# Optimization experiments

Hardware: AMD Instinct MI355X
Metric: run time of the kernel (lower is better)

Reference implementation:

```python
import jax, jax.numpy as jnp
import numpy as np

N = 100000
E = 3200000
NFEAT = 256
NHID = 256
NCLASS = 40


def _uniform(key, shape, stdv):
    return jax.random.uniform(key, shape, jnp.float32, -stdv, stdv)


def setup_inputs() -> dict:
    key = jax.random.key(0)
    ks = jax.random.split(key, 16)
    x = jax.random.normal(ks[0], (N, NFEAT), jnp.float32)
    edge_row = jax.random.randint(ks[1], (E,), 0, N, jnp.int32)
    edge_col = jax.random.randint(ks[2], (E,), 0, N, jnp.int32)
    edge_weight = jax.random.uniform(ks[3], (E,), jnp.float32)
    # MyLinear init: stdv = 1/sqrt(out_features)
    dims = [(NFEAT, NHID), (NHID, NHID), (NHID, NHID), (NHID, NCLASS)]
    params = {}
    for i, (fi, fo) in enumerate(dims):
        stdv = 1.0 / np.sqrt(fo)
        params[f"W{i+1}"] = _uniform(ks[4 + 2 * i], (fi, fo), stdv)
        params[f"b{i+1}"] = _uniform(ks[5 + 2 * i], (fo,), stdv)
    return dict(x=x, edge_row=edge_row, edge_col=edge_col, edge_weight=edge_weight, **params)


def _spmm(edge_row, edge_col, edge_weight, x):
    # out[i] = sum_{(i,j) in E} w_ij * x[j]
    msgs = edge_weight[:, None] * x[edge_col]  # [E, d]
    return jax.ops.segment_sum(msgs, edge_row, num_segments=N)


def reference(x, edge_row, edge_col, edge_weight, W1, b1, W2, b2, W3, b3, W4, b4):
    # layer 0 (ix % mlp_layers == 0 -> residual + spmm)
    h = x + _spmm(edge_row, edge_col, edge_weight, x)
    h = jax.nn.relu(h @ W1 + b1)
    # layer 1
    h = jax.nn.relu(h @ W2 + b2)
    # layer 2 (spmm + residual again)
    h = h + _spmm(edge_row, edge_col, edge_weight, h)
    h = jax.nn.relu(h @ W3 + b3)
    # layer 3 (final, no relu)
    h = h @ W4 + b4
    return jax.nn.log_softmax(h, axis=1)
```

## Files before the change

### kernel.cpp

```cpp
#include <hip/hip_runtime.h>
#include <hip/hip_bf16.h>
#include <cstdint>

#define N_NODES 100000
#define N_EDGES 3200000
#define NFEAT   256
#define NCLASS  40

#define BROWS_LOG 7
#define BROWS     128
#define NBUCK     782
#define CHUNK     8192
#define NBLK      391
#define GHN       (NBUCK * NBLK)

typedef __bf16 bf16;
typedef __attribute__((ext_vector_type(8))) __bf16 bf16x8;
typedef __attribute__((ext_vector_type(4))) float f32x4;
typedef __attribute__((ext_vector_type(2))) float f32x2;

__device__ inline float b2f(unsigned short u) {
    union { unsigned int i; float f; } x; x.i = ((unsigned int)u) << 16; return x.f;
}
__device__ inline unsigned short f2b(float f) {
    union { float f; unsigned int i; } x; x.f = f;
    unsigned int i = x.i;
    return (unsigned short)((i + 0x7fffu + ((i >> 16) & 1u)) >> 16);
}
__device__ inline f32x2 unpack2(unsigned int d) {
    union { unsigned int i; float f; } lo, hi;
    lo.i = d << 16;
    hi.i = d & 0xFFFF0000u;
    return (f32x2){lo.f, hi.f};
}
__device__ inline unsigned int pack2(f32x2 a) {
    return ((unsigned int)f2b(a[0])) | (((unsigned int)f2b(a[1])) << 16);
}

__global__ void prep_w_kernel(const float* __restrict__ W1, const float* __restrict__ W2,
                              const float* __restrict__ W3, const float* __restrict__ W4,
                              unsigned short* __restrict__ WT1, unsigned short* __restrict__ WT2,
                              unsigned short* __restrict__ WT3, unsigned short* __restrict__ WT4) {
    int i = blockIdx.x * blockDim.x + threadIdx.x;
    if (i < 256 * 256) {
        int nIdx = i >> 8, k = i & 255;
        WT1[i] = f2b(W1[k * 256 + nIdx]);
        WT2[i] = f2b(W2[k * 256 + nIdx]);
        WT3[i] = f2b(W3[k * 256 + nIdx]);
    }
    if (i < 48 * 256) {
        int nIdx = i >> 8, k = i & 255;
        WT4[i] = (nIdx < NCLASS) ? f2b(W4[k * NCLASS + nIdx]) : (unsigned short)0;
    }
}

__global__ void cast_kernel(const float* __restrict__ X, unsigned short* __restrict__ Y, int n4) {
    int i = blockIdx.x * blockDim.x + threadIdx.x;
    if (i >= n4) return;
    float4 v = *(const float4*)(X + (size_t)i * 4);
    ushort4 o;
    o.x = f2b(v.x); o.y = f2b(v.y); o.z = f2b(v.z); o.w = f2b(v.w);
    *(ushort4*)(Y + (size_t)i * 4) = o;
}

__global__ __launch_bounds__(256) void p1a_kernel(const int* __restrict__ erow,
                                                  int* __restrict__ ghist) {
    __shared__ int h[NBUCK];
    for (int j = threadIdx.x; j < NBUCK; j += 256) h[j] = 0;
    __syncthreads();
    int base = blockIdx.x * CHUNK;
    for (int j = 0; j < CHUNK; j += 256) {
        int i = base + j + threadIdx.x;
        if (i < N_EDGES) atomicAdd(&h[erow[i] >> BROWS_LOG], 1);
    }
    __syncthreads();
    for (int j = threadIdx.x; j < NBUCK; j += 256)
        ghist[(size_t)j * NBLK + blockIdx.x] = h[j];
}

__global__ void scanB_blocks_kernel(int* __restrict__ g, int* __restrict__ bsums, int n) {
    __shared__ int s[1024];
    int i = blockIdx.x * 1024 + threadIdx.x;
    int v = (i < n) ? g[i] : 0;
    s[threadIdx.x] = v;
    __syncthreads();
    for (int off = 1; off < 1024; off <<= 1) {
        int t = (threadIdx.x >= off) ? s[threadIdx.x - off] : 0;
        __syncthreads();
        s[threadIdx.x] += t;
        __syncthreads();
    }
    if (i < n) g[i] = s[threadIdx.x] - v;
    if (threadIdx.x == 1023) bsums[blockIdx.x] = s[1023];
}

__global__ void scanB_sums_kernel(int* __restrict__ bsums, int nb) {
    __shared__ int s[512];
    int v = (threadIdx.x < nb) ? bsums[threadIdx.x] : 0;
    s[threadIdx.x] = v;
    __syncthreads();
    for (int off = 1; off < 512; off <<= 1) {
        int t = (threadIdx.x >= off) ? s[threadIdx.x - off] : 0;
        __syncthreads();
        s[threadIdx.x] += t;
        __syncthreads();
    }
    if (threadIdx.x < nb) bsums[threadIdx.x] = s[threadIdx.x] - v;
}

__global__ void scanB_add_kernel(int* __restrict__ g, const int* __restrict__ bsums, int n) {
    int i = blockIdx.x * blockDim.x + threadIdx.x;
    if (i < n) g[i] += bsums[i >> 10];
}

__global__ __launch_bounds__(256) void p1c_kernel(const int* __restrict__ erow,
                                                  const int* __restrict__ ecol,
                                                  const float* __restrict__ ew,
                                                  const int* __restrict__ ghist,
                                                  uint2* __restrict__ stage) {
    __shared__ int cur[NBUCK];
    for (int j = threadIdx.x; j < NBUCK; j += 256)
        cur[j] = ghist[(size_t)j * NBLK + blockIdx.x];
    __syncthreads();
    int base = blockIdx.x * CHUNK;
    for (int j = 0; j < CHUNK; j += 1024) {
        int r[4], c[4]; float w[4]; bool m[4];
#pragma unroll
        for (int q = 0; q < 4; q++) {
            int i = base + j + q * 256 + threadIdx.x;
            m[q] = (i < N_EDGES);
            if (m[q]) { r[q] = erow[i]; c[q] = ecol[i]; w[q] = ew[i]; }
        }
#pragma unroll
        for (int q = 0; q < 4; q++) {
            if (m[q]) {
                unsigned int qq = (unsigned int)(w[q] * 32768.f + 0.5f);
                if (qq > 32767u) qq = 32767u;
                int p = atomicAdd(&cur[r[q] >> BROWS_LOG], 1);
                stage[p] = make_uint2((unsigned int)r[q], (((unsigned int)c[q]) << 15) | qq);
            }
        }
    }
}

__global__ __launch_bounds__(256) void p2_kernel(const int* __restrict__ ghist,
                                                 const uint2* __restrict__ stage,
                                                 unsigned int* __restrict__ edges,
                                                 int* __restrict__ rowptr) {
    __shared__ int h[BROWS], sc[BROWS], lcur[BROWS];
    int b = blockIdx.x;
    int lo = ghist[(size_t)b * NBLK];
    int hi = (b + 1 < NBUCK) ? ghist[(size_t)(b + 1) * NBLK] : N_EDGES;
    if (threadIdx.x < BROWS) h[threadIdx.x] = 0;
    __syncthreads();
    for (int i = lo + threadIdx.x; i < hi; i += 256)
        atomicAdd(&h[stage[i].x & (BROWS - 1)], 1);
    __syncthreads();
    if (threadIdx.x < BROWS) sc[threadIdx.x] = h[threadIdx.x];
    __syncthreads();
    for (int off = 1; off < BROWS; off <<= 1) {
        int t = 0;
        if (threadIdx.x < BROWS && threadIdx.x >= off) t = sc[threadIdx.x - off];
        __syncthreads();
        if (threadIdx.x < BROWS) sc[threadIdx.x] += t;
        __syncthreads();
    }
    if (threadIdx.x < BROWS) {
        int ex = sc[threadIdx.x] - h[threadIdx.x];
        int row = b * BROWS + threadIdx.x;
        if (row <= N_NODES) rowptr[row] = lo + ex;
        lcur[threadIdx.x] = lo + ex;
    }
    __syncthreads();
    for (int i = lo + threadIdx.x; i < hi; i += 256) {
        uint2 sd = stage[i];
        int p = atomicAdd(&lcur[sd.x & (BROWS - 1)], 1);
        edges[p] = sd.y;
    }
}

__global__ void spmm_res_kernel(const unsigned short* __restrict__ X, unsigned short* __restrict__ Y,
                                const int* __restrict__ rowptr, const unsigned int* __restrict__ edges,
                                int n) {
    int gtid = blockIdx.x * blockDim.x + threadIdx.x;
    int row = gtid >> 6;
    int lane = gtid & 63;
    if (row >= n) return;
    const int half = lane >> 5;
    const int fb = (lane & 31) * 8;

    f32x2 acc[4];
    {
        uint4 xb = *(const uint4*)(X + (size_t)row * NFEAT + fb);
        if (half == 0) {
            acc[0] = unpack2(xb.x); acc[1] = unpack2(xb.y);
            acc[2] = unpack2(xb.z); acc[3] = unpack2(xb.w);
        } else {
            acc[0] = (f32x2){0.f, 0.f}; acc[1] = (f32x2){0.f, 0.f};
            acc[2] = (f32x2){0.f, 0.f}; acc[3] = (f32x2){0.f, 0.f};
        }
    }

    int s = rowptr[row], e = rowptr[row + 1];
    for (int k = s; k < e; k += 12) {
        int   c[6];
        f32x2 w2[6];
#pragma unroll
        for (int j = 0; j < 6; j++) {
            int kj = k + j * 2 + half;
            int kc = (kj < e) ? kj : (e - 1);
            unsigned int d = edges[kc];
            c[j] = (int)(d >> 15);
            float w = (kj < e) ? (float)(d & 32767u) * (1.f / 32768.f) : 0.f;
            w2[j] = (f32x2){w, w};
        }
        uint4 v[6];
#pragma unroll
        for (int j = 0; j < 6; j++) v[j] = *(const uint4*)(X + (size_t)c[j] * NFEAT + fb);
#pragma unroll
        for (int j = 0; j < 6; j++) {
            acc[0] += w2[j] * unpack2(v[j].x);
            acc[1] += w2[j] * unpack2(v[j].y);
            acc[2] += w2[j] * unpack2(v[j].z);
            acc[3] += w2[j] * unpack2(v[j].w);
        }
    }

#pragma unroll
    for (int i = 0; i < 4; i++) {
        acc[i][0] += __shfl_xor(acc[i][0], 32, 64);
        acc[i][1] += __shfl_xor(acc[i][1], 32, 64);
    }
    if (half == 0) {
        uint4 o;
        o.x = pack2(acc[0]); o.y = pack2(acc[1]);
        o.z = pack2(acc[2]); o.w = pack2(acc[3]);
        *(uint4*)(Y + (size_t)row * NFEAT + fb) = o;
    }
}

template <int NT>
__global__ __launch_bounds__(256) void gemm_relu_kernel(
    const bf16* __restrict__ X, const bf16* __restrict__ WT,
    const float* __restrict__ bias,
    unsigned short* __restrict__ Y, int M) {
    constexpr int NROWS = NT * 16;
    __shared__ unsigned int sB[NROWS * 20];
    const int tid = threadIdx.x;
    const int wave = tid >> 6;
    const int lane = tid & 63;
    const int m = lane & 15;
    const int quad = lane >> 4;
    const int rowBase = blockIdx.x * 64 + wave * 16;
    int arow = rowBase + m;
    if (arow >= M) arow = M - 1;

    f32x4 acc[NT];
#pragma unroll
    for (int t = 0; t < NT; t++) acc[t] = (f32x4){0.f, 0.f, 0.f, 0.f};

    const bf16* xp = X + (size_t)arow * NFEAT + quad * 8;
#pragma unroll
    for (int k0 = 0; k0 < NFEAT; k0 += 32) {
#pragma unroll
        for (int f = tid; f < NROWS * 4; f += 256) {
            int n = f >> 2, j = f & 3;
            uint4 v = *(const uint4*)(WT + (size_t)n * NFEAT + k0 + j * 8);
            *(uint4*)&sB[n * 20 + j * 4] = v;
        }
        __syncthreads();
        bf16x8 a = *(const bf16x8*)(xp + k0);
#pragma unroll
        for (int t = 0; t < NT; t++) {
            bf16x8 b = *(const bf16x8*)&sB[(t * 16 + m) * 20 + quad * 4];
            acc[t] = __builtin_amdgcn_mfma_f32_16x16x32_bf16(a, b, acc[t], 0, 0, 0);
        }
        __syncthreads();
    }

#pragma unroll
    for (int t = 0; t < NT; t++) {
        int col = t * 16 + m;
        float bv = bias[col];
#pragma unroll
        for (int r = 0; r < 4; r++) {
            int row = rowBase + quad * 4 + r;
            if (row < M) {
                float v = fmaxf(acc[t][r] + bv, 0.f);
                Y[(size_t)row * NFEAT + col] = f2b(v);
            }
        }
    }
}

__global__ __launch_bounds__(256) void gemm_ls_kernel(
    const bf16* __restrict__ X, const bf16* __restrict__ WT,
    const float* __restrict__ bias,
    float* __restrict__ out, int M) {
    constexpr int NT = 3;
    constexpr int NROWS = NT * 16;
    __shared__ unsigned int sB[NROWS * 20];
    const int tid = threadIdx.x;
    const int wave = tid >> 6;
    const int lane = tid & 63;
    const int m = lane & 15;
    const int quad = lane >> 4;
    const int rowBase = blockIdx.x * 64 + wave * 16;
    int arow = rowBase + m;
    if (arow >= M) arow = M - 1;

    f32x4 acc[NT];
#pragma unroll
    for (int t = 0; t < NT; t++) acc[t] = (f32x4){0.f, 0.f, 0.f, 0.f};

    const bf16* xp = X + (size_t)arow * NFEAT + quad * 8;
#pragma unroll
    for (int k0 = 0; k0 < NFEAT; k0 += 32) {
        if (tid < NROWS * 4) {
            int n = tid >> 2, j = tid & 3;
            uint4 v = *(const uint4*)(WT + (size_t)n * NFEAT + k0 + j * 8);
            *(uint4*)&sB[n * 20 + j * 4] = v;
        }
        __syncthreads();
        bf16x8 a = *(const bf16x8*)(xp + k0);
#pragma unroll
        for (int t = 0; t < NT; t++) {
            bf16x8 b = *(const bf16x8*)&sB[(t * 16 + m) * 20 + quad * 4];
            acc[t] = __builtin_amdgcn_mfma_f32_16x16x32_bf16(a, b, acc[t], 0, 0, 0);
        }
        __syncthreads();
    }

    float v[3][4];
    bool valid[3];
#pragma unroll
    for (int t = 0; t < 3; t++) {
        int col = t * 16 + m;
        valid[t] = (col < NCLASS);
        float bv = valid[t] ? bias[col] : 0.f;
#pragma unroll
        for (int r = 0; r < 4; r++) v[t][r] = acc[t][r] + bv;
    }

#pragma unroll
    for (int r = 0; r < 4; r++) {
        int row = rowBase + quad * 4 + r;
        float mx = -1e30f;
#pragma unroll
        for (int t = 0; t < 3; t++) if (valid[t]) mx = fmaxf(mx, v[t][r]);
#pragma unroll
        for (int off = 1; off < 16; off <<= 1) mx = fmaxf(mx, __shfl_xor(mx, off, 64));
        float sm = 0.f;
#pragma unroll
        for (int t = 0; t < 3; t++) if (valid[t]) sm += __expf(v[t][r] - mx);
#pragma unroll
        for (int off = 1; off < 16; off <<= 1) sm += __shfl_xor(sm, off, 64);
        float ls = __logf(sm);
        if (row < M) {
#pragma unroll
            for (int t = 0; t < 3; t++) {
                int col = t * 16 + m;
                if (col < NCLASS)
                    out[(size_t)row * NCLASS + col] = v[t][r] - mx - ls;
            }
        }
    }
}

extern "C" void kernel_launch(void* const* d_in, const int* in_sizes, int n_in,
                              void* d_out, int out_size, void* d_ws, size_t ws_size,
                              hipStream_t stream) {
    const float* x   = (const float*)d_in[0];
    const int* erow  = (const int*)d_in[1];
    const int* ecol  = (const int*)d_in[2];
    const float* ew  = (const float*)d_in[3];
    const float* W1  = (const float*)d_in[4];
    const float* W2  = (const float*)d_in[6];
    const float* W3  = (const float*)d_in[8];
    const float* W4  = (const float*)d_in[10];
    const float* b1  = (const float*)d_in[5];
    const float* b2  = (const float*)d_in[7];
    const float* b3  = (const float*)d_in[9];
    const float* b4  = (const float*)d_in[11];

    char* ws = (char*)d_ws;
    size_t off = 0;
    auto alloc = [&](size_t bytes) -> char* {
        char* p = ws + off;
        off = (off + bytes + 255) & ~(size_t)255;
        return p;
    };
    int* rowptr  = (int*)alloc((size_t)(N_NODES + 1) * 4);
    int* bsumsB  = (int*)alloc(512 * 4);
    unsigned int* edges = (unsigned int*)alloc((size_t)N_EDGES * 4);
    int* ghist   = (int*)alloc((size_t)GHN * 4);
    unsigned short* WT1 = (unsigned short*)alloc(256 * 256 * 2);
    unsigned short* WT2 = (unsigned short*)alloc(256 * 256 * 2);
    unsigned short* WT3 = (unsigned short*)alloc(256 * 256 * 2);
    unsigned short* WT4 = (unsigned short*)alloc(48 * 256 * 2);
    unsigned short* hA  = (unsigned short*)alloc((size_t)N_NODES * NFEAT * 2);
    uint2* stage        = (uint2*)hA;
    unsigned short* hB  = (unsigned short*)d_in[0];
    (void)ws_size; (void)n_in; (void)in_sizes; (void)out_size;

    prep_w_kernel<<<(256 * 256 + 255) / 256, 256, 0, stream>>>(
        W1, W2, W3, W4, WT1, WT2, WT3, WT4);
    p1a_kernel<<<NBLK, 256, 0, stream>>>(erow, ghist);
    int nsb = (GHN + 1023) / 1024;
    scanB_blocks_kernel<<<nsb, 1024, 0, stream>>>(ghist, bsumsB, GHN);
    scanB_sums_kernel<<<1, 512, 0, stream>>>(bsumsB, nsb);
    scanB_add_kernel<<<(GHN + 255) / 256, 256, 0, stream>>>(ghist, bsumsB, GHN);
    p1c_kernel<<<NBLK, 256, 0, stream>>>(erow, ecol, ew, ghist, stage);
    p2_kernel<<<NBUCK, 256, 0, stream>>>(ghist, stage, edges, rowptr);

    const int n4 = N_NODES * NFEAT / 4;
    const int spmm_grid = (N_NODES * 64 + 255) / 256;
    const int gemm_grid = (N_NODES + 63) / 64;

    cast_kernel<<<(n4 + 255) / 256, 256, 0, stream>>>(x, hA, n4);
    spmm_res_kernel<<<spmm_grid, 256, 0, stream>>>(hA, hB, rowptr, edges, N_NODES);
    gemm_relu_kernel<16><<<gemm_grid, 256, 0, stream>>>(
        (const bf16*)hB, (const bf16*)WT1, b1, hB, N_NODES);
    gemm_relu_kernel<16><<<gemm_grid, 256, 0, stream>>>(
        (const bf16*)hB, (const bf16*)WT2, b2, hB, N_NODES);
    spmm_res_kernel<<<spmm_grid, 256, 0, stream>>>(hB, hA, rowptr, edges, N_NODES);
    gemm_relu_kernel<16><<<gemm_grid, 256, 0, stream>>>(
        (const bf16*)hA, (const bf16*)WT3, b3, hA, N_NODES);
    gemm_ls_kernel<<<gemm_grid, 256, 0, stream>>>(
        (const bf16*)hA, (const bf16*)WT4, b4, (float*)d_out, N_NODES);
}
```

Before: 969.6 us.

## Fuse SpMM gather with subsequent GEMM layers via shared-memory tiles

Merges each SpMM-with-residual with its following dense layers into one kernel. Each 64-row block gathers neighbor features into LDS, then runs the MFMA GEMMs from LDS and keeps the intermediate activations there. This removes global writes and reads of full activation matrices and four kernel launches. The gather now runs 16 rows sequentially per wave, and the larger LDS footprint lowers occupancy, which may reduce latency hiding for the random gathers.

```diff
diff --git a/kernel.cpp b/kernel.cpp
--- a/kernel.cpp
+++ b/kernel.cpp
@@ -13,6 +13,8 @@
 #define CHUNK     8192
 #define NBLK      391
 #define GHN       (NBUCK * NBLK)
+
+#define SAP 264
 
 typedef __bf16 bf16;
 typedef __attribute__((ext_vector_type(8))) __bf16 bf16x8;
@@ -179,112 +181,137 @@
     }
 }
 
-__global__ void spmm_res_kernel(const unsigned short* __restrict__ X, unsigned short* __restrict__ Y,
-                                const int* __restrict__ rowptr, const unsigned int* __restrict__ edges,
-                                int n) {
-    int gtid = blockIdx.x * blockDim.x + threadIdx.x;
-    int row = gtid >> 6;
-    int lane = gtid & 63;
-    if (row >= n) return;
+
+__device__ __forceinline__ void gather64(
+    const unsigned short* __restrict__ X,
+    const int* __restrict__ rowptr,
+    const unsigned int* __restrict__ edges,
+    unsigned short* __restrict__ sA,
+    int blockRow, int M, int wave, int lane)
+{
     const int half = lane >> 5;
     const int fb = (lane & 31) * 8;
-
-    f32x2 acc[4];
-    {
-        uint4 xb = *(const uint4*)(X + (size_t)row * NFEAT + fb);
-        if (half == 0) {
-            acc[0] = unpack2(xb.x); acc[1] = unpack2(xb.y);
-            acc[2] = unpack2(xb.z); acc[3] = unpack2(xb.w);
-        } else {
-            acc[0] = (f32x2){0.f, 0.f}; acc[1] = (f32x2){0.f, 0.f};
-            acc[2] = (f32x2){0.f, 0.f}; acc[3] = (f32x2){0.f, 0.f};
-        }
-    }
-
-    int s = rowptr[row], e = rowptr[row + 1];
-    for (int k = s; k < e; k += 12) {
-        int   c[6];
-        f32x2 w2[6];
-#pragma unroll
-        for (int j = 0; j < 6; j++) {
-            int kj = k + j * 2 + half;
-            int kc = (kj < e) ? kj : (e - 1);
-            unsigned int d = edges[kc];
-            c[j] = (int)(d >> 15);
-            float w = (kj < e) ? (float)(d & 32767u) * (1.f / 32768.f) : 0.f;
-            w2[j] = (f32x2){w, w};
-        }
-        uint4 v[6];
-#pragma unroll
-        for (int j = 0; j < 6; j++) v[j] = *(const uint4*)(X + (size_t)c[j] * NFEAT + fb);
-#pragma unroll
-        for (int j = 0; j < 6; j++) {
-            acc[0] += w2[j] * unpack2(v[j].x);
-            acc[1] += w2[j] * unpack2(v[j].y);
-            acc[2] += w2[j] * unpack2(v[j].z);
-            acc[3] += w2[j] * unpack2(v[j].w);
-        }
-    }
-
-#pragma unroll
-    for (int i = 0; i < 4; i++) {
-        acc[i][0] += __shfl_xor(acc[i][0], 32, 64);
-        acc[i][1] += __shfl_xor(acc[i][1], 32, 64);
-    }
-    if (half == 0) {
-        uint4 o;
-        o.x = pack2(acc[0]); o.y = pack2(acc[1]);
-        o.z = pack2(acc[2]); o.w = pack2(acc[3]);
-        *(uint4*)(Y + (size_t)row * NFEAT + fb) = o;
-    }
-}
-
-template <int NT>
-__global__ __launch_bounds__(256) void gemm_relu_kernel(
-    const bf16* __restrict__ X, const bf16* __restrict__ WT,
-    const float* __restrict__ bias,
-    unsigned short* __restrict__ Y, int M) {
-    constexpr int NROWS = NT * 16;
-    __shared__ unsigned int sB[NROWS * 20];
-    const int tid = threadIdx.x;
-    const int wave = tid >> 6;
-    const int lane = tid & 63;
-    const int m = lane & 15;
-    const int quad = lane >> 4;
-    const int rowBase = blockIdx.x * 64 + wave * 16;
-    int arow = rowBase + m;
-    if (arow >= M) arow = M - 1;
-
-    f32x4 acc[NT];
-#pragma unroll
-    for (int t = 0; t < NT; t++) acc[t] = (f32x4){0.f, 0.f, 0.f, 0.f};
-
-    const bf16* xp = X + (size_t)arow * NFEAT + quad * 8;
+    for (int lr = 0; lr < 16; ++lr) {
+        const int lrow = wave * 16 + lr;
+        const int row = blockRow + lrow;
+        if (row < M) {
+            f32x2 acc[4];
+            uint4 xb = *(const uint4*)(X + (size_t)row * NFEAT + fb);
+            if (half == 0) {
+                acc[0] = unpack2(xb.x); acc[1] = unpack2(xb.y);
+                acc[2] = unpack2(xb.z); acc[3] = unpack2(xb.w);
+            } else {
+                acc[0] = (f32x2){0.f, 0.f}; acc[1] = (f32x2){0.f, 0.f};
+                acc[2] = (f32x2){0.f, 0.f}; acc[3] = (f32x2){0.f, 0.f};
+            }
+            int s = rowptr[row], e = rowptr[row + 1];
+            for (int k = s; k < e; k += 12) {
+                int   c[6];
+                f32x2 w2[6];
+#pragma unroll
+                for (int j = 0; j < 6; j++) {
+                    int kj = k + j * 2 + half;
+                    int kc = (kj < e) ? kj : (e - 1);
+                    unsigned int d = edges[kc];
+                    c[j] = (int)(d >> 15);
+                    float w = (kj < e) ? (float)(d & 32767u) * (1.f / 32768.f) : 0.f;
+                    w2[j] = (f32x2){w, w};
+                }
+                uint4 v[6];
+#pragma unroll
+                for (int j = 0; j < 6; j++) v[j] = *(const uint4*)(X + (size_t)c[j] * NFEAT + fb);
+#pragma unroll
+                for (int j = 0; j < 6; j++) {
+                    acc[0] += w2[j] * unpack2(v[j].x);
+                    acc[1] += w2[j] * unpack2(v[j].y);
+                    acc[2] += w2[j] * unpack2(v[j].z);
+                    acc[3] += w2[j] * unpack2(v[j].w);
+                }
+            }
+#pragma unroll
+            for (int i = 0; i < 4; i++) {
+                acc[i][0] += __shfl_xor(acc[i][0], 32, 64);
+                acc[i][1] += __shfl_xor(acc[i][1], 32, 64);
+            }
+            if (half == 0) {
+                uint4 o;
+                o.x = pack2(acc[0]); o.y = pack2(acc[1]);
+                o.z = pack2(acc[2]); o.w = pack2(acc[3]);
+                *(uint4*)&sA[lrow * SAP + fb] = o;
+            }
+        } else if (half == 0) {
+            uint4 z; z.x = 0u; z.y = 0u; z.z = 0u; z.w = 0u;
+            *(uint4*)&sA[lrow * SAP + fb] = z;
+        }
+    }
+}
+
+__device__ __forceinline__ void gemm256(
+    const unsigned short* __restrict__ sA,
+    unsigned int* __restrict__ sB,
+    const unsigned short* __restrict__ WT,
+    f32x4 acc[16], int wave, int m, int quad, int tid)
+{
+#pragma unroll
+    for (int t = 0; t < 16; t++) acc[t] = (f32x4){0.f, 0.f, 0.f, 0.f};
 #pragma unroll
     for (int k0 = 0; k0 < NFEAT; k0 += 32) {
 #pragma unroll
-        for (int f = tid; f < NROWS * 4; f += 256) {
+        for (int f = tid; f < 1024; f += 256) {
             int n = f >> 2, j = f & 3;
             uint4 v = *(const uint4*)(WT + (size_t)n * NFEAT + k0 + j * 8);
             *(uint4*)&sB[n * 20 + j * 4] = v;
         }
         __syncthreads();
-        bf16x8 a = *(const bf16x8*)(xp + k0);
-#pragma unroll
-        for (int t = 0; t < NT; t++) {
+        bf16x8 a = *(const bf16x8*)&sA[(wave * 16 + m) * SAP + k0 + quad * 8];
+#pragma unroll
+        for (int t = 0; t < 16; t++) {
             bf16x8 b = *(const bf16x8*)&sB[(t * 16 + m) * 20 + quad * 4];
             acc[t] = __builtin_amdgcn_mfma_f32_16x16x32_bf16(a, b, acc[t], 0, 0, 0);
         }
         __syncthreads();
     }
-
-#pragma unroll
-    for (int t = 0; t < NT; t++) {
+}
+
+__global__ __launch_bounds__(256, 3) void fused_mlp_kernel(
+    const unsigned short* __restrict__ X,
+    const int* __restrict__ rowptr, const unsigned int* __restrict__ edges,
+    const unsigned short* __restrict__ WT1, const float* __restrict__ b1,
+    const unsigned short* __restrict__ WT2, const float* __restrict__ b2,
+    unsigned short* __restrict__ Y,
+    int M)
+{
+    __shared__ unsigned short sA[64 * SAP];
+    __shared__ unsigned int sB[256 * 20];
+    const int tid = threadIdx.x;
+    const int wave = tid >> 6, lane = tid & 63;
+    const int blockRow = blockIdx.x * 64;
+
+    gather64(X, rowptr, edges, sA, blockRow, M, wave, lane);
+
+    const int m = lane & 15, quad = lane >> 4;
+    f32x4 acc[16];
+
+    gemm256(sA, sB, WT1, acc, wave, m, quad, tid);
+#pragma unroll
+    for (int t = 0; t < 16; t++) {
         int col = t * 16 + m;
-        float bv = bias[col];
+        float bv = b1[col];
 #pragma unroll
         for (int r = 0; r < 4; r++) {
-            int row = rowBase + quad * 4 + r;
+            float v = fmaxf(acc[t][r] + bv, 0.f);
+            sA[(wave * 16 + quad * 4 + r) * SAP + col] = f2b(v);
+        }
+    }
+
+    gemm256(sA, sB, WT2, acc, wave, m, quad, tid);
+#pragma unroll
+    for (int t = 0; t < 16; t++) {
+        int col = t * 16 + m;
+        float bv = b2[col];
+#pragma unroll
+        for (int r = 0; r < 4; r++) {
+            int row = blockRow + wave * 16 + quad * 4 + r;
             if (row < M) {
                 float v = fmaxf(acc[t][r] + bv, 0.f);
                 Y[(size_t)row * NFEAT + col] = f2b(v);
@@ -293,40 +320,52 @@
     }
 }
 
-__global__ __launch_bounds__(256) void gemm_ls_kernel(
-    const bf16* __restrict__ X, const bf16* __restrict__ WT,
-    const float* __restrict__ bias,
-    float* __restrict__ out, int M) {
-    constexpr int NT = 3;
-    constexpr int NROWS = NT * 16;
-    __shared__ unsigned int sB[NROWS * 20];
+__global__ __launch_bounds__(256, 3) void fused_out_kernel(
+    const unsigned short* __restrict__ X,
+    const int* __restrict__ rowptr, const unsigned int* __restrict__ edges,
+    const unsigned short* __restrict__ WT3, const float* __restrict__ b3,
+    const unsigned short* __restrict__ WT4, const float* __restrict__ b4,
+    float* __restrict__ out, int M)
+{
+    __shared__ unsigned short sA[64 * SAP];
+    __shared__ unsigned int sB[256 * 20];
     const int tid = threadIdx.x;
-    const int wave = tid >> 6;
-    const int lane = tid & 63;
-    const int m = lane & 15;
-    const int quad = lane >> 4;
-    const int rowBase = blockIdx.x * 64 + wave * 16;
-    int arow = rowBase + m;
-    if (arow >= M) arow = M - 1;
-
-    f32x4 acc[NT];
-#pragma unroll
-    for (int t = 0; t < NT; t++) acc[t] = (f32x4){0.f, 0.f, 0.f, 0.f};
-
-    const bf16* xp = X + (size_t)arow * NFEAT + quad * 8;
+    const int wave = tid >> 6, lane = tid & 63;
+    const int blockRow = blockIdx.x * 64;
+
+    gather64(X, rowptr, edges, sA, blockRow, M, wave, lane);
+
+    const int m = lane & 15, quad = lane >> 4;
+    f32x4 acc[16];
+
+    gemm256(sA, sB, WT3, acc, wave, m, quad, tid);
+#pragma unroll
+    for (int t = 0; t < 16; t++) {
+        int col = t * 16 + m;
+        float bv = b3[col];
+#pragma unroll
+        for (int r = 0; r < 4; r++) {
+            float v = fmaxf(acc[t][r] + bv, 0.f);
+            sA[(wave * 16 + quad * 4 + r) * SAP + col] = f2b(v);
+        }
+    }
+
+    f32x4 a4[3];
+#pragma unroll
+    for (int t = 0; t < 3; t++) a4[t] = (f32x4){0.f, 0.f, 0.f, 0.f};
 #pragma unroll
     for (int k0 = 0; k0 < NFEAT; k0 += 32) {
-        if (tid < NROWS * 4) {
+        if (tid < 192) {
             int n = tid >> 2, j = tid & 3;
-            uint4 v = *(const uint4*)(WT + (size_t)n * NFEAT + k0 + j * 8);
+            uint4 v = *(const uint4*)(WT4 + (size_t)n * NFEAT + k0 + j * 8);
             *(uint4*)&sB[n * 20 + j * 4] = v;
         }
         __syncthreads();
-        bf16x8 a = *(const bf16x8*)(xp + k0);
-#pragma unroll
-        for (int t = 0; t < NT; t++) {
+        bf16x8 a = *(const bf16x8*)&sA[(wave * 16 + m) * SAP + k0 + quad * 8];
+#pragma unroll
+        for (int t = 0; t < 3; t++) {
             bf16x8 b = *(const bf16x8*)&sB[(t * 16 + m) * 20 + quad * 4];
-            acc[t] = __builtin_amdgcn_mfma_f32_16x16x32_bf16(a, b, acc[t], 0, 0, 0);
+            a4[t] = __builtin_amdgcn_mfma_f32_16x16x32_bf16(a, b, a4[t], 0, 0, 0);
         }
         __syncthreads();
     }
@@ -337,14 +376,14 @@
     for (int t = 0; t < 3; t++) {
         int col = t * 16 + m;
         valid[t] = (col < NCLASS);
-        float bv = valid[t] ? bias[col] : 0.f;
-#pragma unroll
-        for (int r = 0; r < 4; r++) v[t][r] = acc[t][r] + bv;
+        float bv = valid[t] ? b4[col] : 0.f;
+#pragma unroll
+        for (int r = 0; r < 4; r++) v[t][r] = a4[t][r] + bv;
     }
 
 #pragma unroll
     for (int r = 0; r < 4; r++) {
-        int row = rowBase + quad * 4 + r;
+        int row = blockRow + wave * 16 + quad * 4 + r;
         float mx = -1e30f;
 #pragma unroll
         for (int t = 0; t < 3; t++) if (valid[t]) mx = fmaxf(mx, v[t][r]);
@@ -414,18 +453,11 @@
     p2_kernel<<<NBUCK, 256, 0, stream>>>(ghist, stage, edges, rowptr);
 
     const int n4 = N_NODES * NFEAT / 4;
-    const int spmm_grid = (N_NODES * 64 + 255) / 256;
-    const int gemm_grid = (N_NODES + 63) / 64;
+    const int grid64 = (N_NODES + 63) / 64;
 
     cast_kernel<<<(n4 + 255) / 256, 256, 0, stream>>>(x, hA, n4);
-    spmm_res_kernel<<<spmm_grid, 256, 0, stream>>>(hA, hB, rowptr, edges, N_NODES);
-    gemm_relu_kernel<16><<<gemm_grid, 256, 0, stream>>>(
-        (const bf16*)hB, (const bf16*)WT1, b1, hB, N_NODES);
-    gemm_relu_kernel<16><<<gemm_grid, 256, 0, stream>>>(
-        (const bf16*)hB, (const bf16*)WT2, b2, hB, N_NODES);
-    spmm_res_kernel<<<spmm_grid, 256, 0, stream>>>(hB, hA, rowptr, edges, N_NODES);
-    gemm_relu_kernel<16><<<gemm_grid, 256, 0, stream>>>(
-        (const bf16*)hA, (const bf16*)WT3, b3, hA, N_NODES);
-    gemm_ls_kernel<<<gemm_grid, 256, 0, stream>>>(
-        (const bf16*)hA, (const bf16*)WT4, b4, (float*)d_out, N_NODES);
-}
+    fused_mlp_kernel<<<grid64, 256, 0, stream>>>(
+        hA, rowptr, edges, WT1, b1, WT2, b2, hB, N_NODES);
+    fused_out_kernel<<<grid64, 256, 0, stream>>>(
+        hB, rowptr, edges, WT3, b3, WT4, b4, (float*)d_out, N_NODES);
+}
```

Result: slower. 989.6 us (+2.1%).

## Make GEMM kernels persistent with full weight matrix resident in LDS

Applied to the files above, without the earlier changes.

The relu GEMMs become persistent kernels: 256 blocks of 512 threads each load the whole 256x256 bf16 weight matrix into padded LDS once, then loop over 128-row tiles. Each wave preloads its full A row slice into registers before the MFMA loop. This removes the per-k-step weight reloads and the barriers inside the k loop. The log-softmax GEMM also loads all its weights once per block. In exchange, about 135 KB of dynamic LDS per block limits residency to one block per CU, and the in-place write to hB/hA relies on each tile reading its rows before writing them.

```diff
diff --git a/kernel.cpp b/kernel.cpp
--- a/kernel.cpp
+++ b/kernel.cpp
@@ -13,6 +13,9 @@
 #define CHUNK     8192
 #define NBLK      391
 #define GHN       (NBUCK * NBLK)
+
+#define GP 264
+#define GEMM_TILES 782
 
 typedef __bf16 bf16;
 typedef __attribute__((ext_vector_type(8))) __bf16 bf16x8;
@@ -239,96 +242,94 @@
     }
 }
 
-template <int NT>
-__global__ __launch_bounds__(256) void gemm_relu_kernel(
-    const bf16* __restrict__ X, const bf16* __restrict__ WT,
-    const float* __restrict__ bias,
-    unsigned short* __restrict__ Y, int M) {
-    constexpr int NROWS = NT * 16;
-    __shared__ unsigned int sB[NROWS * 20];
+__global__ __launch_bounds__(512) void gemm_relu_persist_kernel(
+    const bf16* __restrict__ X, const unsigned short* __restrict__ WT,
+    const float* __restrict__ bias, unsigned short* __restrict__ Y, int M) {
+    extern __shared__ unsigned short sW[];
     const int tid = threadIdx.x;
     const int wave = tid >> 6;
     const int lane = tid & 63;
     const int m = lane & 15;
     const int quad = lane >> 4;
-    const int rowBase = blockIdx.x * 64 + wave * 16;
-    int arow = rowBase + m;
-    if (arow >= M) arow = M - 1;
-
-    f32x4 acc[NT];
-#pragma unroll
-    for (int t = 0; t < NT; t++) acc[t] = (f32x4){0.f, 0.f, 0.f, 0.f};
-
-    const bf16* xp = X + (size_t)arow * NFEAT + quad * 8;
-#pragma unroll
-    for (int k0 = 0; k0 < NFEAT; k0 += 32) {
-#pragma unroll
-        for (int f = tid; f < NROWS * 4; f += 256) {
-            int n = f >> 2, j = f & 3;
-            uint4 v = *(const uint4*)(WT + (size_t)n * NFEAT + k0 + j * 8);
-            *(uint4*)&sB[n * 20 + j * 4] = v;
-        }
-        __syncthreads();
-        bf16x8 a = *(const bf16x8*)(xp + k0);
-#pragma unroll
-        for (int t = 0; t < NT; t++) {
-            bf16x8 b = *(const bf16x8*)&sB[(t * 16 + m) * 20 + quad * 4];
-            acc[t] = __builtin_amdgcn_mfma_f32_16x16x32_bf16(a, b, acc[t], 0, 0, 0);
-        }
-        __syncthreads();
-    }
-
-#pragma unroll
-    for (int t = 0; t < NT; t++) {
-        int col = t * 16 + m;
-        float bv = bias[col];
-#pragma unroll
-        for (int r = 0; r < 4; r++) {
-            int row = rowBase + quad * 4 + r;
-            if (row < M) {
-                float v = fmaxf(acc[t][r] + bv, 0.f);
-                Y[(size_t)row * NFEAT + col] = f2b(v);
+
+    for (int f = tid; f < 8192; f += 512) {
+        int n = f >> 5, j = f & 31;
+        uint4 v = *(const uint4*)(WT + (size_t)n * NFEAT + j * 8);
+        *(uint4*)&sW[n * GP + j * 8] = v;
+    }
+    float bv[16];
+#pragma unroll
+    for (int t = 0; t < 16; t++) bv[t] = bias[t * 16 + m];
+    __syncthreads();
+
+    for (int tile = blockIdx.x; tile < GEMM_TILES; tile += gridDim.x) {
+        const int rowBase = tile * 128 + wave * 16;
+        int arow = rowBase + m;
+        if (arow >= M) arow = M - 1;
+        const bf16* xp = X + (size_t)arow * NFEAT + quad * 8;
+        bf16x8 a[8];
+#pragma unroll
+        for (int k = 0; k < 8; k++) a[k] = *(const bf16x8*)(xp + k * 32);
+        f32x4 acc[16];
+#pragma unroll
+        for (int t = 0; t < 16; t++) acc[t] = (f32x4){0.f, 0.f, 0.f, 0.f};
+#pragma unroll
+        for (int k = 0; k < 8; k++) {
+#pragma unroll
+            for (int t = 0; t < 16; t++) {
+                bf16x8 b = *(const bf16x8*)&sW[(t * 16 + m) * GP + k * 32 + quad * 8];
+                acc[t] = __builtin_amdgcn_mfma_f32_16x16x32_bf16(a[k], b, acc[t], 0, 0, 0);
             }
         }
-    }
-}
-
-__global__ __launch_bounds__(256) void gemm_ls_kernel(
-    const bf16* __restrict__ X, const bf16* __restrict__ WT,
-    const float* __restrict__ bias,
-    float* __restrict__ out, int M) {
-    constexpr int NT = 3;
-    constexpr int NROWS = NT * 16;
-    __shared__ unsigned int sB[NROWS * 20];
+#pragma unroll
+        for (int t = 0; t < 16; t++) {
+            int col = t * 16 + m;
+#pragma unroll
+            for (int r = 0; r < 4; r++) {
+                int row = rowBase + quad * 4 + r;
+                if (row < M) {
+                    float v = fmaxf(acc[t][r] + bv[t], 0.f);
+                    Y[(size_t)row * NFEAT + col] = f2b(v);
+                }
+            }
+        }
+    }
+}
+
+__global__ __launch_bounds__(512) void gemm_ls_persist_kernel(
+    const bf16* __restrict__ X, const unsigned short* __restrict__ WT,
+    const float* __restrict__ bias, float* __restrict__ out, int M) {
+    __shared__ unsigned short sW[48 * GP];
     const int tid = threadIdx.x;
     const int wave = tid >> 6;
     const int lane = tid & 63;
     const int m = lane & 15;
     const int quad = lane >> 4;
-    const int rowBase = blockIdx.x * 64 + wave * 16;
+
+    for (int f = tid; f < 1536; f += 512) {
+        int n = f >> 5, j = f & 31;
+        uint4 v = *(const uint4*)(WT + (size_t)n * NFEAT + j * 8);
+        *(uint4*)&sW[n * GP + j * 8] = v;
+    }
+    __syncthreads();
+
+    const int rowBase = blockIdx.x * 128 + wave * 16;
     int arow = rowBase + m;
     if (arow >= M) arow = M - 1;
-
-    f32x4 acc[NT];
-#pragma unroll
-    for (int t = 0; t < NT; t++) acc[t] = (f32x4){0.f, 0.f, 0.f, 0.f};
-
     const bf16* xp = X + (size_t)arow * NFEAT + quad * 8;
-#pragma unroll
-    for (int k0 = 0; k0 < NFEAT; k0 += 32) {
-        if (tid < NROWS * 4) {
-            int n = tid >> 2, j = tid & 3;
-            uint4 v = *(const uint4*)(WT + (size_t)n * NFEAT + k0 + j * 8);
-            *(uint4*)&sB[n * 20 + j * 4] = v;
-        }
-        __syncthreads();
-        bf16x8 a = *(const bf16x8*)(xp + k0);
-#pragma unroll
-        for (int t = 0; t < NT; t++) {
-            bf16x8 b = *(const bf16x8*)&sB[(t * 16 + m) * 20 + quad * 4];
-            acc[t] = __builtin_amdgcn_mfma_f32_16x16x32_bf16(a, b, acc[t], 0, 0, 0);
-        }
-        __syncthreads();
+    bf16x8 a[8];
+#pragma unroll
+    for (int k = 0; k < 8; k++) a[k] = *(const bf16x8*)(xp + k * 32);
+    f32x4 acc[3];
+#pragma unroll
+    for (int t = 0; t < 3; t++) acc[t] = (f32x4){0.f, 0.f, 0.f, 0.f};
+#pragma unroll
+    for (int k = 0; k < 8; k++) {
+#pragma unroll
+        for (int t = 0; t < 3; t++) {
+            bf16x8 b = *(const bf16x8*)&sW[(t * 16 + m) * GP + k * 32 + quad * 8];
+            acc[t] = __builtin_amdgcn_mfma_f32_16x16x32_bf16(a[k], b, acc[t], 0, 0, 0);
+        }
     }
 
     float v[3][4];
@@ -337,9 +338,9 @@
     for (int t = 0; t < 3; t++) {
         int col = t * 16 + m;
         valid[t] = (col < NCLASS);
-        float bv = valid[t] ? bias[col] : 0.f;
-#pragma unroll
-        for (int r = 0; r < 4; r++) v[t][r] = acc[t][r] + bv;
+        float bvv = valid[t] ? bias[col] : 0.f;
+#pragma unroll
+        for (int r = 0; r < 4; r++) v[t][r] = acc[t][r] + bvv;
     }
 
 #pragma unroll
@@ -415,17 +416,17 @@
 
     const int n4 = N_NODES * NFEAT / 4;
     const int spmm_grid = (N_NODES * 64 + 255) / 256;
-    const int gemm_grid = (N_NODES + 63) / 64;
+    const size_t gemm_lds = (size_t)256 * GP * 2;
 
     cast_kernel<<<(n4 + 255) / 256, 256, 0, stream>>>(x, hA, n4);
     spmm_res_kernel<<<spmm_grid, 256, 0, stream>>>(hA, hB, rowptr, edges, N_NODES);
-    gemm_relu_kernel<16><<<gemm_grid, 256, 0, stream>>>(
-        (const bf16*)hB, (const bf16*)WT1, b1, hB, N_NODES);
-    gemm_relu_kernel<16><<<gemm_grid, 256, 0, stream>>>(
-        (const bf16*)hB, (const bf16*)WT2, b2, hB, N_NODES);
+    gemm_relu_persist_kernel<<<256, 512, gemm_lds, stream>>>(
+        (const bf16*)hB, WT1, b1, hB, N_NODES);
+    gemm_relu_persist_kernel<<<256, 512, gemm_lds, stream>>>(
+        (const bf16*)hB, WT2, b2, hB, N_NODES);
     spmm_res_kernel<<<spmm_grid, 256, 0, stream>>>(hB, hA, rowptr, edges, N_NODES);
-    gemm_relu_kernel<16><<<gemm_grid, 256, 0, stream>>>(
-        (const bf16*)hA, (const bf16*)WT3, b3, hA, N_NODES);
-    gemm_ls_kernel<<<gemm_grid, 256, 0, stream>>>(
-        (const bf16*)hA, (const bf16*)WT4, b4, (float*)d_out, N_NODES);
-}
+    gemm_relu_persist_kernel<<<256, 512, gemm_lds, stream>>>(
+        (const bf16*)hA, WT3, b3, hA, N_NODES);
+    gemm_ls_persist_kernel<<<GEMM_TILES, 512, 0, stream>>>(
+        (const bf16*)hA, WT4, b4, (float*)d_out, N_NODES);
+}
```

Result: slower. 1.451 ms (+49.6%).
